# Optimization experiments

Measured on AMD Instinct MI355X. Metric: run time of the kernel, lower is better.

## Reference

```python
import jax, jax.numpy as jnp
import numpy as np

NEG_SLOPE = 0.2
NEG_INF = -1e9


def _gat_branch(x, src, dst, edge_type, t, W, a_src, a_dst, b):
    """Single-head PyG GATConv restricted (by masking) to edges with edge_type == t,
    with self-loops added (PyG default add_self_loops=True)."""
    N = x.shape[0]
    h = x @ W                                   # [N, out_dim]
    s = h @ a_src                               # [N] source attention term
    d = h @ a_dst                               # [N] destination attention term
    # real edges (masked by type)
    e_edge = jax.nn.leaky_relu(s[src] + d[dst], NEG_SLOPE)
    e_edge = jnp.where(edge_type == t, e_edge, NEG_INF)
    # self-loop edges i -> i
    e_self = jax.nn.leaky_relu(s + d, NEG_SLOPE)
    dst_all = jnp.concatenate([dst, jnp.arange(N)])          # [E+N]
    e_all = jnp.concatenate([e_edge, e_self])                 # [E+N]
    # softmax over incoming edges per destination node (segment softmax)
    m = jax.ops.segment_max(e_all, dst_all, num_segments=N)
    p = jnp.exp(e_all - m[dst_all])
    denom = jax.ops.segment_sum(p, dst_all, num_segments=N)
    alpha = p / denom[dst_all]                                 # [E+N]
    msg = jnp.concatenate([h[src], h], axis=0) * alpha[:, None]
    return jax.ops.segment_sum(msg, dst_all, num_segments=N) + b


def setup_inputs() -> dict:
    key = jax.random.key(0)
    ks = jax.random.split(key, 12)
    N, E, in_dim, out_dim = 100000, 1000000, 64, 64
    glorot = (6.0 / (in_dim + out_dim)) ** 0.5
    att = (6.0 / (1 + out_dim)) ** 0.5
    return {
        "x": jax.random.normal(ks[0], (N, in_dim), dtype=jnp.float32),
        "edge_index": jax.random.randint(ks[1], (2, E), 0, N),
        "edge_type": jax.random.randint(ks[2], (E,), 0, 2),
        "W_login": jax.random.uniform(ks[3], (in_dim, out_dim), jnp.float32, -glorot, glorot),
        "a_src_login": jax.random.uniform(ks[4], (out_dim,), jnp.float32, -att, att),
        "a_dst_login": jax.random.uniform(ks[5], (out_dim,), jnp.float32, -att, att),
        "b_login": jnp.zeros((out_dim,), jnp.float32),
        "W_exec": jax.random.uniform(ks[6], (in_dim, out_dim), jnp.float32, -glorot, glorot),
        "a_src_exec": jax.random.uniform(ks[7], (out_dim,), jnp.float32, -att, att),
        "a_dst_exec": jax.random.uniform(ks[8], (out_dim,), jnp.float32, -att, att),
        "b_exec": jnp.zeros((out_dim,), jnp.float32),
    }


def reference(x, edge_index, edge_type, W_login, a_src_login, a_dst_login, b_login,
              W_exec, a_src_exec, a_dst_exec, b_exec):
    src, dst = edge_index[0], edge_index[1]
    out = _gat_branch(x, src, dst, edge_type, 0, W_login, a_src_login, a_dst_login, b_login)
    out = out + _gat_branch(x, src, dst, edge_type, 1, W_exec, a_src_exec, a_dst_exec, b_exec)
    return out
```

## Files before the change

### kernel.cpp

```cpp
#include <hip/hip_runtime.h>

#define D 64
#define CAP 896
#define BINB 256

typedef unsigned short u16;
typedef __attribute__((ext_vector_type(8))) __bf16 bf16x8;
typedef __attribute__((ext_vector_type(4))) float f32x4;

__device__ __forceinline__ float lrelu(float x) { return x > 0.f ? x : 0.2f * x; }
__device__ __forceinline__ u16 f2bf(float f) {
    unsigned u = __float_as_uint(f);
    return (u16)((u + 0x7fffu + ((u >> 16) & 1u)) >> 16);
}
__device__ __forceinline__ float bf2f(u16 v) { return __uint_as_float((unsigned)v << 16); }
__device__ __forceinline__ unsigned pack2(float lo, float hi) {
    return (unsigned)f2bf(lo) | ((unsigned)f2bf(hi) << 16);
}
__device__ __forceinline__ float blo(unsigned u) { return __uint_as_float(u << 16); }
__device__ __forceinline__ float bhi(unsigned u) { return __uint_as_float(u & 0xffff0000u); }

__global__ __launch_bounds__(256) void k_gemm3(
    const float* __restrict__ x,
    const float* __restrict__ W0, const float* __restrict__ as0, const float* __restrict__ ad0,
    const float* __restrict__ W1, const float* __restrict__ as1, const float* __restrict__ ad1,
    u16* __restrict__ hb, float* __restrict__ s_tab, float* __restrict__ d_tab,
    int N, int ntiles)
{
    __shared__ u16 Wb[2][64][64];
    __shared__ u16 Xb[64][72];
    __shared__ float wsd[4][64];

    const int tid = threadIdx.x;

    for (int i = tid; i < 4096; i += 256) {
        const int k = i >> 6, n = i & 63;
        Wb[0][n][k] = f2bf(W0[i]);
        Wb[1][n][k] = f2bf(W1[i]);
    }
    {
        const int k = tid & 63;
        const int v = tid >> 6;
        const float* Ws = (v < 2) ? W0 : W1;
        const float* av = (v == 0) ? as0 : (v == 1) ? ad0 : (v == 2) ? as1 : ad1;
        float q = 0.f;
        for (int n = 0; n < 64; ++n) q = fmaf(Ws[(k << 6) + n], av[n], q);
        wsd[v][k] = q;
    }
    __syncthreads();

    const int lane = tid & 63;
    const int nl = lane & 15, quad = lane >> 4;
    const int wv = tid >> 6;

    bf16x8 bfrag[2][4][2];
#pragma unroll
    for (int br = 0; br < 2; ++br)
#pragma unroll
        for (int t = 0; t < 4; ++t)
#pragma unroll
            for (int h = 0; h < 2; ++h)
                bfrag[br][t][h] = *(const bf16x8*)&Wb[br][t * 16 + nl][h * 32 + quad * 8];

    const int rstage = tid >> 2;
    const int kc = (tid & 3) << 4;

    for (int tile = blockIdx.x; tile < ntiles; tile += gridDim.x) {
        const long n0 = (long)tile << 6;
        __syncthreads();
        {
            long row = n0 + rstage; if (row >= N) row = N - 1;
            const float4* xp = (const float4*)(x + row * D + kc);
            const float4 v0 = xp[0], v1 = xp[1], v2 = xp[2], v3 = xp[3];

            unsigned q[8];
            q[0] = pack2(v0.x, v0.y); q[1] = pack2(v0.z, v0.w);
            q[2] = pack2(v1.x, v1.y); q[3] = pack2(v1.z, v1.w);
            q[4] = pack2(v2.x, v2.y); q[5] = pack2(v2.z, v2.w);
            q[6] = pack2(v3.x, v3.y); q[7] = pack2(v3.z, v3.w);
            *(uint4*)&Xb[rstage][kc]     = make_uint4(q[0], q[1], q[2], q[3]);
            *(uint4*)&Xb[rstage][kc + 8] = make_uint4(q[4], q[5], q[6], q[7]);

            float ps[4];
#pragma unroll
            for (int v = 0; v < 4; ++v) {
                const float4* wp = (const float4*)&wsd[v][kc];
                const float4 wa = wp[0], wb = wp[1], wc = wp[2], wd = wp[3];
                float s = 0.f;
                s = fmaf(v0.x, wa.x, s); s = fmaf(v0.y, wa.y, s);
                s = fmaf(v0.z, wa.z, s); s = fmaf(v0.w, wa.w, s);
                s = fmaf(v1.x, wb.x, s); s = fmaf(v1.y, wb.y, s);
                s = fmaf(v1.z, wb.z, s); s = fmaf(v1.w, wb.w, s);
                s = fmaf(v2.x, wc.x, s); s = fmaf(v2.y, wc.y, s);
                s = fmaf(v2.z, wc.z, s); s = fmaf(v2.w, wc.w, s);
                s = fmaf(v3.x, wd.x, s); s = fmaf(v3.y, wd.y, s);
                s = fmaf(v3.z, wd.z, s); s = fmaf(v3.w, wd.w, s);
                ps[v] = s;
            }
#pragma unroll
            for (int v = 0; v < 4; ++v) {
                ps[v] += __shfl_xor(ps[v], 1, 64);
                ps[v] += __shfl_xor(ps[v], 2, 64);
            }
            const long rw = n0 + rstage;
            if ((tid & 3) == 0 && rw < N) {
                s_tab[(rw << 1)]     = ps[0]; d_tab[(rw << 1)]     = ps[1];
                s_tab[(rw << 1) | 1] = ps[2]; d_tab[(rw << 1) | 1] = ps[3];
            }
        }
        __syncthreads();

        const int rbase = wv << 4;
        const bf16x8 a0 = *(const bf16x8*)&Xb[rbase + nl][quad * 8];
        const bf16x8 a1 = *(const bf16x8*)&Xb[rbase + nl][32 + quad * 8];

        f32x4 acc[2][4];
#pragma unroll
        for (int br = 0; br < 2; ++br)
#pragma unroll
            for (int t = 0; t < 4; ++t) {
                f32x4 c = {0.f, 0.f, 0.f, 0.f};
                c = __builtin_amdgcn_mfma_f32_16x16x32_bf16(a0, bfrag[br][t][0], c, 0, 0, 0);
                c = __builtin_amdgcn_mfma_f32_16x16x32_bf16(a1, bfrag[br][t][1], c, 0, 0, 0);
                acc[br][t] = c;
            }

#pragma unroll
        for (int reg = 0; reg < 4; ++reg) {
            const long row = n0 + rbase + (quad << 2) + reg;
            if (row < N) {
#pragma unroll
                for (int br = 0; br < 2; ++br) {
                    uint2 v;
                    v.x = pack2(acc[br][0][reg], acc[br][1][reg]);
                    v.y = pack2(acc[br][2][reg], acc[br][3][reg]);
                    *(uint2*)(hb + (((row << 1) | br) << 6) + (nl << 2)) = v;
                }
            }
        }
    }
}

__global__ __launch_bounds__(256) void k_bin1(
    const int* __restrict__ src, const int* __restrict__ dst,
    const int* __restrict__ et, int* __restrict__ bktcnt,
    unsigned* __restrict__ bkt, int E, int nbk, int Eseg)
{
    extern __shared__ int cnt_l[];
    const int tid = threadIdx.x;
    for (int i = tid; i < nbk; i += 256) cnt_l[i] = 0;
    __syncthreads();

    const long e0 = (long)blockIdx.x * Eseg;
    const long e1 = min(e0 + (long)Eseg, (long)E);

    long i = e0 + tid;
    for (; i + 256 * 7 < e1; i += 256 * 8) {
        int d[8];
#pragma unroll
        for (int k = 0; k < 8; ++k) d[k] = dst[i + 256 * k];
#pragma unroll
        for (int k = 0; k < 8; ++k) atomicAdd(&cnt_l[d[k] >> 6], 1);
    }
    for (; i < e1; i += 256) atomicAdd(&cnt_l[dst[i] >> 6], 1);
    __syncthreads();

    for (int j = tid; j < nbk; j += 256) {
        const int c = cnt_l[j];
        cnt_l[j] = c ? atomicAdd(bktcnt + j, c) : 0;
    }
    __syncthreads();

    i = e0 + tid;
    for (; i + 256 * 7 < e1; i += 256 * 8) {
        int d[8];
#pragma unroll
        for (int k = 0; k < 8; ++k) d[k] = dst[i + 256 * k];
#pragma unroll
        for (int k = 0; k < 8; ++k) {
            const int bb = d[k] >> 6;
            const long ii = i + 256 * k;
            const int slot = atomicAdd(&cnt_l[bb], 1);
            if (slot < CAP)
                bkt[(long)bb * CAP + slot] =
                    ((unsigned)(d[k] & 63) << 18) | ((unsigned)src[ii] << 1) | (unsigned)et[ii];
        }
    }
    for (; i < e1; i += 256) {
        const int d = dst[i];
        const int bb = d >> 6;
        const int slot = atomicAdd(&cnt_l[bb], 1);
        if (slot < CAP)
            bkt[(long)bb * CAP + slot] =
                ((unsigned)(d & 63) << 18) | ((unsigned)src[i] << 1) | (unsigned)et[i];
    }
}

__global__ __launch_bounds__(512) void k_proc(
    const int* __restrict__ bktcnt, const unsigned* __restrict__ bkt,
    const float* __restrict__ s_tab, const float* __restrict__ d_tab,
    const u16* __restrict__ hb,
    const float* __restrict__ b0, const float* __restrict__ b1,
    float* __restrict__ out, int N)
{
    __shared__ unsigned tok[CAP];
    __shared__ int degl[64];
    __shared__ int curl[64];
    __shared__ float bsum[64];

    const int tid = threadIdx.x;
    const int b = blockIdx.x;
    const int lo = b << 6;
    const int cnt_nodes = min(64, N - lo);
    const int nb = min(bktcnt[b], CAP);

    if (tid < 64) { degl[tid] = 0; bsum[tid] = b0[tid] + b1[tid]; }
    __syncthreads();

    unsigned pr[2];
    int ns = 0;
    for (int i = tid; i < nb; i += 512) {
        const unsigned p = bkt[(long)b * CAP + i];
        pr[ns++] = p;
        atomicAdd(&degl[(p >> 18) & 63], 1);
    }
    __syncthreads();
    if (tid < 64) {
        int v = degl[tid];
        const int orig = v;
#pragma unroll
        for (int o = 1; o < 64; o <<= 1) {
            const int u = __shfl_up(v, o, 64);
            if (tid >= o) v += u;
        }
        curl[tid] = v - orig;
    }
    __syncthreads();
    for (int k = 0, i = tid; k < ns; i += 512, ++k) {
        const unsigned p = pr[k];
        const int s = atomicAdd(&curl[(p >> 18) & 63], 1);
        tok[s] = p & 0x3FFFFu;
    }
    __syncthreads();

    const int lane = tid & 63;
    const int wave = tid >> 6;
    const int q = lane >> 4;
    const int cl = lane & 15;

    for (int ni = wave; ni < cnt_nodes; ni += 8) {
        const int n = lo + ni;
        const int deg = degl[ni];
        const int off = curl[ni] - deg;
        const float d0n = d_tab[(n << 1)];
        const float d1n = d_tab[(n << 1) | 1];

        if (deg <= 62) {
            const int cnt = deg + 2;
            unsigned cmb = 0; unsigned t = 0; float e = 0.f;
            if (lane < deg) {
                cmb = tok[off + lane];
                t = cmb & 1u;
                e = lrelu(s_tab[cmb] + (t ? d1n : d0n));
            } else if (lane == deg)   { cmb = (unsigned)(n << 1);      t = 0; e = lrelu(s_tab[cmb] + d0n); }
            else if (lane == deg + 1) { cmb = (unsigned)(n << 1) | 1u; t = 1; e = lrelu(s_tab[cmb] + d1n); }

            const bool act = lane < cnt;
            const float p = act ? __expf(e) : 0.f;
            float p0 = t ? 0.f : p;
            float p1 = t ? p : 0.f;
#pragma unroll
            for (int o = 32; o; o >>= 1) {
                p0 += __shfl_xor(p0, o, 64);
                p1 += __shfl_xor(p1, o, 64);
            }
            const float a_r = act ? p / (t ? p1 : p0) : 0.f;

            float4 acc = {0.f, 0.f, 0.f, 0.f};
            const int nq = (cnt + 3) >> 2;
            int pp = 0;
            for (; pp + 1 < nq; pp += 2) {
                const int iA = (pp << 2) + q;
                const int iB = iA + 4;
                const int iBc = iB < cnt ? iB : cnt - 1;
                float aA    = __shfl(a_r, iA, 64);
                unsigned cA = __shfl(cmb, iA, 64);
                float aB    = __shfl(a_r, iBc, 64);
                unsigned cB = __shfl(cmb, iBc, 64);
                if (iB >= cnt) aB = 0.f;
                const uint2 uA = *(const uint2*)(hb + ((long)cA << 6) + (cl << 2));
                const uint2 uB = *(const uint2*)(hb + ((long)cB << 6) + (cl << 2));
                acc.x = fmaf(aA, blo(uA.x), acc.x);
                acc.y = fmaf(aA, bhi(uA.x), acc.y);
                acc.z = fmaf(aA, blo(uA.y), acc.z);
                acc.w = fmaf(aA, bhi(uA.y), acc.w);
                acc.x = fmaf(aB, blo(uB.x), acc.x);
                acc.y = fmaf(aB, bhi(uB.x), acc.y);
                acc.z = fmaf(aB, blo(uB.y), acc.z);
                acc.w = fmaf(aB, bhi(uB.y), acc.w);
            }
            if (pp < nq) {
                const int iA = (pp << 2) + q;
                const int iAc = iA < cnt ? iA : cnt - 1;
                float aA    = __shfl(a_r, iAc, 64);
                unsigned cA = __shfl(cmb, iAc, 64);
                if (iA >= cnt) aA = 0.f;
                const uint2 uA = *(const uint2*)(hb + ((long)cA << 6) + (cl << 2));
                acc.x = fmaf(aA, blo(uA.x), acc.x);
                acc.y = fmaf(aA, bhi(uA.x), acc.y);
                acc.z = fmaf(aA, blo(uA.y), acc.z);
                acc.w = fmaf(aA, bhi(uA.y), acc.w);
            }
            acc.x += __shfl_xor(acc.x, 16, 64);
            acc.y += __shfl_xor(acc.y, 16, 64);
            acc.z += __shfl_xor(acc.z, 16, 64);
            acc.w += __shfl_xor(acc.w, 16, 64);
            acc.x += __shfl_xor(acc.x, 32, 64);
            acc.y += __shfl_xor(acc.y, 32, 64);
            acc.z += __shfl_xor(acc.z, 32, 64);
            acc.w += __shfl_xor(acc.w, 32, 64);
            if (lane < 16) {
                float* op = out + ((long)n << 6);
                op[cl]      = acc.x + bsum[cl];
                op[16 + cl] = acc.y + bsum[16 + cl];
                op[32 + cl] = acc.z + bsum[32 + cl];
                op[48 + cl] = acc.w + bsum[48 + cl];
            }
        } else {
            const int oc = ((lane & 3) << 4) + (lane >> 2);
            const float es0 = lrelu(s_tab[(n << 1)] + d0n);
            const float es1 = lrelu(s_tab[(n << 1) | 1] + d1n);
            float p0 = 0.f, p1 = 0.f;
            for (int j = lane; j < deg; j += 64) {
                const unsigned c = tok[off + j];
                const float e = lrelu(s_tab[c] + ((c & 1u) ? d1n : d0n));
                if (c & 1u) p1 += __expf(e); else p0 += __expf(e);
            }
#pragma unroll
            for (int o = 32; o; o >>= 1) {
                p0 += __shfl_xor(p0, o, 64);
                p1 += __shfl_xor(p1, o, 64);
            }
            const float den0 = p0 + __expf(es0);
            const float den1 = p1 + __expf(es1);

            float acc = (__expf(es0) / den0) * bf2f(hb[((long)n << 7) + lane])
                      + (__expf(es1) / den1) * bf2f(hb[((long)n << 7) + 64 + lane]);
            for (int base = 0; base < deg; base += 64) {
                const int j = base + lane;
                unsigned ck = 0; float a = 0.f;
                if (j < deg) {
                    ck = tok[off + j];
                    const float e = lrelu(s_tab[ck] + ((ck & 1u) ? d1n : d0n));
                    a = __expf(e) / ((ck & 1u) ? den1 : den0);
                }
                const int lim = min(64, deg - base);
                for (int jj = 0; jj < lim; ++jj) {
                    const float aj = __shfl(a, jj, 64);
                    const unsigned cj = __shfl(ck, jj, 64);
                    acc = fmaf(aj, bf2f(hb[((long)cj << 6) + lane]), acc);
                }
            }
            out[((long)n << 6) + oc] = acc + bsum[oc];
        }
    }
}

extern "C" void kernel_launch(void* const* d_in, const int* in_sizes, int n_in,
                              void* d_out, int out_size, void* d_ws, size_t ws_size,
                              hipStream_t stream) {
    const float* x   = (const float*)d_in[0];
    const int*   ei  = (const int*)d_in[1];
    const int*   et  = (const int*)d_in[2];
    const float* W0  = (const float*)d_in[3];
    const float* as0 = (const float*)d_in[4];
    const float* ad0 = (const float*)d_in[5];
    const float* b0  = (const float*)d_in[6];
    const float* W1  = (const float*)d_in[7];
    const float* as1 = (const float*)d_in[8];
    const float* ad1 = (const float*)d_in[9];
    const float* b1  = (const float*)d_in[10];
    float* out = (float*)d_out;

    const int N = in_sizes[0] / D;
    const int E = in_sizes[1] / 2;
    const int* src = ei;
    const int* dst = ei + E;

    const int nbk = (N + 63) >> 6;

    char* w = (char*)d_ws;
    u16* hb = (u16*)w;            w += (size_t)2 * N * D * sizeof(u16);
    float* s_tab = (float*)w;     w += (size_t)2 * N * sizeof(float);
    float* d_tab = (float*)w;     w += (size_t)2 * N * sizeof(float);
    int* bktcnt = (int*)w;        w += (size_t)nbk * sizeof(int);
    unsigned* bkt = (unsigned*)w; w += (size_t)nbk * CAP * sizeof(unsigned);

    const int ntiles = (N + 63) / 64;
    const int Eseg = (E + BINB - 1) / BINB;

    hipMemsetAsync(bktcnt, 0, (size_t)nbk * sizeof(int), stream);
    k_gemm3<<<768, 256, 0, stream>>>(x, W0, as0, ad0, W1, as1, ad1,
                                     hb, s_tab, d_tab, N, ntiles);
    k_bin1<<<BINB, 256, (size_t)nbk * sizeof(int), stream>>>(
        src, dst, et, bktcnt, bkt, E, nbk, Eseg);
    k_proc<<<nbk, 512, 0, stream>>>(bktcnt, bkt, s_tab, d_tab, hb, b0, b1, out, N);
}
```

Measured before the change: 195.1 us.

## Fuse GEMM and edge binning into one launch; precompute per-edge softmax weights in LDS

Merges the GEMM and binning kernels into one grid, so binning blocks run alongside GEMM blocks and one launch is saved. The bin histogram is chunked by BINCH, which makes binning blocks rescan their edge segment several times. In k_proc, self-loops become extra tokens, and each edge's exp weight and per-node denominators are computed once into shared memory with atomics. The high-degree path is removed and every node uses the vectorized gather loop. Risks are extra passes over edges during binning and shared-memory atomic contention on the denominators.

```diff
diff --git a/kernel.cpp b/kernel.cpp
--- a/kernel.cpp
+++ b/kernel.cpp
@@ -3,6 +3,8 @@
 #define D 64
 #define CAP 896
 #define BINB 256
+#define GEMMB 768
+#define BINCH 1600
 
 typedef unsigned short u16;
 typedef __attribute__((ext_vector_type(8))) __bf16 bf16x8;
@@ -13,25 +15,95 @@
     unsigned u = __float_as_uint(f);
     return (u16)((u + 0x7fffu + ((u >> 16) & 1u)) >> 16);
 }
-__device__ __forceinline__ float bf2f(u16 v) { return __uint_as_float((unsigned)v << 16); }
 __device__ __forceinline__ unsigned pack2(float lo, float hi) {
     return (unsigned)f2bf(lo) | ((unsigned)f2bf(hi) << 16);
 }
 __device__ __forceinline__ float blo(unsigned u) { return __uint_as_float(u << 16); }
 __device__ __forceinline__ float bhi(unsigned u) { return __uint_as_float(u & 0xffff0000u); }
 
-__global__ __launch_bounds__(256) void k_gemm3(
+struct SG { u16 Wb[2][64][64]; u16 Xb[64][72]; float wsd[4][64]; };
+struct SB { int cnt[BINCH]; };
+
+__global__ __launch_bounds__(256) void k_gb(
     const float* __restrict__ x,
     const float* __restrict__ W0, const float* __restrict__ as0, const float* __restrict__ ad0,
     const float* __restrict__ W1, const float* __restrict__ as1, const float* __restrict__ ad1,
     u16* __restrict__ hb, float* __restrict__ s_tab, float* __restrict__ d_tab,
-    int N, int ntiles)
+    int N, int ntiles,
+    const int* __restrict__ src, const int* __restrict__ dst, const int* __restrict__ et,
+    int* __restrict__ bktcnt, unsigned* __restrict__ bkt, int E, int nbk, int Eseg)
 {
-    __shared__ u16 Wb[2][64][64];
-    __shared__ u16 Xb[64][72];
-    __shared__ float wsd[4][64];
-
+    __shared__ union SM { SG g; SB bn; } sm;
     const int tid = threadIdx.x;
+
+    if (blockIdx.x >= GEMMB) {
+        int* cnt_l = sm.bn.cnt;
+        const int blk = blockIdx.x - GEMMB;
+        const long e0 = (long)blk * Eseg;
+        const long e1 = min(e0 + (long)Eseg, (long)E);
+        for (int base = 0; base < nbk; base += BINCH) {
+            const int lim = min(BINCH, nbk - base);
+            for (int i = tid; i < lim; i += 256) cnt_l[i] = 0;
+            __syncthreads();
+            long i = e0 + tid;
+            for (; i + 256 * 7 < e1; i += 256 * 8) {
+                int d8[8];
+#pragma unroll
+                for (int k = 0; k < 8; ++k) d8[k] = dst[i + 256 * k];
+#pragma unroll
+                for (int k = 0; k < 8; ++k) {
+                    const int bb = (d8[k] >> 6) - base;
+                    if ((unsigned)bb < (unsigned)lim) atomicAdd(&cnt_l[bb], 1);
+                }
+            }
+            for (; i < e1; i += 256) {
+                const int bb = (dst[i] >> 6) - base;
+                if ((unsigned)bb < (unsigned)lim) atomicAdd(&cnt_l[bb], 1);
+            }
+            __syncthreads();
+            for (int j = tid; j < lim; j += 256) {
+                const int c = cnt_l[j];
+                cnt_l[j] = c ? atomicAdd(bktcnt + base + j, c) : 0;
+            }
+            __syncthreads();
+            i = e0 + tid;
+            for (; i + 256 * 7 < e1; i += 256 * 8) {
+                int d8[8], s8[8], t8[8];
+#pragma unroll
+                for (int k = 0; k < 8; ++k) d8[k] = dst[i + 256 * k];
+#pragma unroll
+                for (int k = 0; k < 8; ++k) s8[k] = src[i + 256 * k];
+#pragma unroll
+                for (int k = 0; k < 8; ++k) t8[k] = et[i + 256 * k];
+#pragma unroll
+                for (int k = 0; k < 8; ++k) {
+                    const int bb = (d8[k] >> 6) - base;
+                    if ((unsigned)bb < (unsigned)lim) {
+                        const int slot = atomicAdd(&cnt_l[bb], 1);
+                        if (slot < CAP)
+                            bkt[(long)(base + bb) * CAP + slot] =
+                                ((unsigned)(d8[k] & 63) << 18) | ((unsigned)s8[k] << 1) | (unsigned)t8[k];
+                    }
+                }
+            }
+            for (; i < e1; i += 256) {
+                const int d = dst[i];
+                const int bb = (d >> 6) - base;
+                if ((unsigned)bb < (unsigned)lim) {
+                    const int slot = atomicAdd(&cnt_l[bb], 1);
+                    if (slot < CAP)
+                        bkt[(long)(base + bb) * CAP + slot] =
+                            ((unsigned)(d & 63) << 18) | ((unsigned)src[i] << 1) | (unsigned)et[i];
+                }
+            }
+            __syncthreads();
+        }
+        return;
+    }
+
+    auto& Wb  = sm.g.Wb;
+    auto& Xb  = sm.g.Xb;
+    auto& wsd = sm.g.wsd;
 
     for (int i = tid; i < 4096; i += 256) {
         const int k = i >> 6, n = i & 63;
@@ -65,7 +137,7 @@
     const int rstage = tid >> 2;
     const int kc = (tid & 3) << 4;
 
-    for (int tile = blockIdx.x; tile < ntiles; tile += gridDim.x) {
+    for (int tile = blockIdx.x; tile < ntiles; tile += GEMMB) {
         const long n0 = (long)tile << 6;
         __syncthreads();
         {
@@ -141,61 +213,6 @@
     }
 }
 
-__global__ __launch_bounds__(256) void k_bin1(
-    const int* __restrict__ src, const int* __restrict__ dst,
-    const int* __restrict__ et, int* __restrict__ bktcnt,
-    unsigned* __restrict__ bkt, int E, int nbk, int Eseg)
-{
-    extern __shared__ int cnt_l[];
-    const int tid = threadIdx.x;
-    for (int i = tid; i < nbk; i += 256) cnt_l[i] = 0;
-    __syncthreads();
-
-    const long e0 = (long)blockIdx.x * Eseg;
-    const long e1 = min(e0 + (long)Eseg, (long)E);
-
-    long i = e0 + tid;
-    for (; i + 256 * 7 < e1; i += 256 * 8) {
-        int d[8];
-#pragma unroll
-        for (int k = 0; k < 8; ++k) d[k] = dst[i + 256 * k];
-#pragma unroll
-        for (int k = 0; k < 8; ++k) atomicAdd(&cnt_l[d[k] >> 6], 1);
-    }
-    for (; i < e1; i += 256) atomicAdd(&cnt_l[dst[i] >> 6], 1);
-    __syncthreads();
-
-    for (int j = tid; j < nbk; j += 256) {
-        const int c = cnt_l[j];
-        cnt_l[j] = c ? atomicAdd(bktcnt + j, c) : 0;
-    }
-    __syncthreads();
-
-    i = e0 + tid;
-    for (; i + 256 * 7 < e1; i += 256 * 8) {
-        int d[8];
-#pragma unroll
-        for (int k = 0; k < 8; ++k) d[k] = dst[i + 256 * k];
-#pragma unroll
-        for (int k = 0; k < 8; ++k) {
-            const int bb = d[k] >> 6;
-            const long ii = i + 256 * k;
-            const int slot = atomicAdd(&cnt_l[bb], 1);
-            if (slot < CAP)
-                bkt[(long)bb * CAP + slot] =
-                    ((unsigned)(d[k] & 63) << 18) | ((unsigned)src[ii] << 1) | (unsigned)et[ii];
-        }
-    }
-    for (; i < e1; i += 256) {
-        const int d = dst[i];
-        const int bb = d >> 6;
-        const int slot = atomicAdd(&cnt_l[bb], 1);
-        if (slot < CAP)
-            bkt[(long)bb * CAP + slot] =
-                ((unsigned)(d & 63) << 18) | ((unsigned)src[i] << 1) | (unsigned)et[i];
-    }
-}
-
 __global__ __launch_bounds__(512) void k_proc(
     const int* __restrict__ bktcnt, const unsigned* __restrict__ bkt,
     const float* __restrict__ s_tab, const float* __restrict__ d_tab,
@@ -203,9 +220,11 @@
     const float* __restrict__ b0, const float* __restrict__ b1,
     float* __restrict__ out, int N)
 {
-    __shared__ unsigned tok[CAP];
-    __shared__ int degl[64];
-    __shared__ int curl[64];
+    __shared__ uint2 tok2[CAP + 128];
+    __shared__ int   degl[64];
+    __shared__ int   curl[64];
+    __shared__ float den[128];
+    __shared__ float dl[128];
     __shared__ float bsum[64];
 
     const int tid = threadIdx.x;
@@ -214,11 +233,18 @@
     const int cnt_nodes = min(64, N - lo);
     const int nb = min(bktcnt[b], CAP);
 
-    if (tid < 64) { degl[tid] = 0; bsum[tid] = b0[tid] + b1[tid]; }
-    __syncthreads();
-
-    unsigned pr[2];
-    int ns = 0;
+    if (tid < 64) {
+        degl[tid] = (lo + tid < N) ? 2 : 0;
+        bsum[tid] = b0[tid] + b1[tid];
+    }
+    if (tid < 128) {
+        den[tid] = 0.f;
+        const int n = lo + (tid >> 1);
+        dl[tid] = (n < N) ? d_tab[(n << 1) | (tid & 1)] : 0.f;
+    }
+    __syncthreads();
+
+    unsigned pr[2]; int ns = 0;
     for (int i = tid; i < nb; i += 512) {
         const unsigned p = bkt[(long)b * CAP + i];
         pr[ns++] = p;
@@ -236,10 +262,26 @@
         curl[tid] = v - orig;
     }
     __syncthreads();
+    if (tid < 2 * cnt_nodes) {
+        const int ni = tid >> 1;
+        const int slot = atomicAdd(&curl[ni], 1);
+        tok2[slot].x = ((unsigned)ni << 18) | ((unsigned)((lo + ni) << 1)) | (unsigned)(tid & 1);
+    }
     for (int k = 0, i = tid; k < ns; i += 512, ++k) {
         const unsigned p = pr[k];
-        const int s = atomicAdd(&curl[(p >> 18) & 63], 1);
-        tok[s] = p & 0x3FFFFu;
+        const int slot = atomicAdd(&curl[(p >> 18) & 63], 1);
+        tok2[slot].x = p;
+    }
+    __syncthreads();
+
+    const int T = nb + (cnt_nodes << 1);
+    for (int j = tid; j < T; j += 512) {
+        const unsigned u = tok2[j].x;
+        const int idx = (int)(((u >> 18) << 1) | (u & 1u));
+        const float e = lrelu(s_tab[u & 0x3FFFFu] + dl[idx]);
+        const float p = __expf(e);
+        tok2[j].y = __float_as_uint(p);
+        atomicAdd(&den[idx], p);
     }
     __syncthreads();
 
@@ -249,119 +291,58 @@
     const int cl = lane & 15;
 
     for (int ni = wave; ni < cnt_nodes; ni += 8) {
-        const int n = lo + ni;
-        const int deg = degl[ni];
-        const int off = curl[ni] - deg;
-        const float d0n = d_tab[(n << 1)];
-        const float d1n = d_tab[(n << 1) | 1];
-
-        if (deg <= 62) {
-            const int cnt = deg + 2;
-            unsigned cmb = 0; unsigned t = 0; float e = 0.f;
-            if (lane < deg) {
-                cmb = tok[off + lane];
-                t = cmb & 1u;
-                e = lrelu(s_tab[cmb] + (t ? d1n : d0n));
-            } else if (lane == deg)   { cmb = (unsigned)(n << 1);      t = 0; e = lrelu(s_tab[cmb] + d0n); }
-            else if (lane == deg + 1) { cmb = (unsigned)(n << 1) | 1u; t = 1; e = lrelu(s_tab[cmb] + d1n); }
-
-            const bool act = lane < cnt;
-            const float p = act ? __expf(e) : 0.f;
-            float p0 = t ? 0.f : p;
-            float p1 = t ? p : 0.f;
-#pragma unroll
-            for (int o = 32; o; o >>= 1) {
-                p0 += __shfl_xor(p0, o, 64);
-                p1 += __shfl_xor(p1, o, 64);
-            }
-            const float a_r = act ? p / (t ? p1 : p0) : 0.f;
-
-            float4 acc = {0.f, 0.f, 0.f, 0.f};
-            const int nq = (cnt + 3) >> 2;
-            int pp = 0;
-            for (; pp + 1 < nq; pp += 2) {
-                const int iA = (pp << 2) + q;
-                const int iB = iA + 4;
-                const int iBc = iB < cnt ? iB : cnt - 1;
-                float aA    = __shfl(a_r, iA, 64);
-                unsigned cA = __shfl(cmb, iA, 64);
-                float aB    = __shfl(a_r, iBc, 64);
-                unsigned cB = __shfl(cmb, iBc, 64);
-                if (iB >= cnt) aB = 0.f;
-                const uint2 uA = *(const uint2*)(hb + ((long)cA << 6) + (cl << 2));
-                const uint2 uB = *(const uint2*)(hb + ((long)cB << 6) + (cl << 2));
-                acc.x = fmaf(aA, blo(uA.x), acc.x);
-                acc.y = fmaf(aA, bhi(uA.x), acc.y);
-                acc.z = fmaf(aA, blo(uA.y), acc.z);
-                acc.w = fmaf(aA, bhi(uA.y), acc.w);
-                acc.x = fmaf(aB, blo(uB.x), acc.x);
-                acc.y = fmaf(aB, bhi(uB.x), acc.y);
-                acc.z = fmaf(aB, blo(uB.y), acc.z);
-                acc.w = fmaf(aB, bhi(uB.y), acc.w);
-            }
-            if (pp < nq) {
-                const int iA = (pp << 2) + q;
-                const int iAc = iA < cnt ? iA : cnt - 1;
-                float aA    = __shfl(a_r, iAc, 64);
-                unsigned cA = __shfl(cmb, iAc, 64);
-                if (iA >= cnt) aA = 0.f;
-                const uint2 uA = *(const uint2*)(hb + ((long)cA << 6) + (cl << 2));
-                acc.x = fmaf(aA, blo(uA.x), acc.x);
-                acc.y = fmaf(aA, bhi(uA.x), acc.y);
-                acc.z = fmaf(aA, blo(uA.y), acc.z);
-                acc.w = fmaf(aA, bhi(uA.y), acc.w);
-            }
-            acc.x += __shfl_xor(acc.x, 16, 64);
-            acc.y += __shfl_xor(acc.y, 16, 64);
-            acc.z += __shfl_xor(acc.z, 16, 64);
-            acc.w += __shfl_xor(acc.w, 16, 64);
-            acc.x += __shfl_xor(acc.x, 32, 64);
-            acc.y += __shfl_xor(acc.y, 32, 64);
-            acc.z += __shfl_xor(acc.z, 32, 64);
-            acc.w += __shfl_xor(acc.w, 32, 64);
-            if (lane < 16) {
-                float* op = out + ((long)n << 6);
-                op[cl]      = acc.x + bsum[cl];
-                op[16 + cl] = acc.y + bsum[16 + cl];
-                op[32 + cl] = acc.z + bsum[32 + cl];
-                op[48 + cl] = acc.w + bsum[48 + cl];
-            }
-        } else {
-            const int oc = ((lane & 3) << 4) + (lane >> 2);
-            const float es0 = lrelu(s_tab[(n << 1)] + d0n);
-            const float es1 = lrelu(s_tab[(n << 1) | 1] + d1n);
-            float p0 = 0.f, p1 = 0.f;
-            for (int j = lane; j < deg; j += 64) {
-                const unsigned c = tok[off + j];
-                const float e = lrelu(s_tab[c] + ((c & 1u) ? d1n : d0n));
-                if (c & 1u) p1 += __expf(e); else p0 += __expf(e);
-            }
-#pragma unroll
-            for (int o = 32; o; o >>= 1) {
-                p0 += __shfl_xor(p0, o, 64);
-                p1 += __shfl_xor(p1, o, 64);
-            }
-            const float den0 = p0 + __expf(es0);
-            const float den1 = p1 + __expf(es1);
-
-            float acc = (__expf(es0) / den0) * bf2f(hb[((long)n << 7) + lane])
-                      + (__expf(es1) / den1) * bf2f(hb[((long)n << 7) + 64 + lane]);
-            for (int base = 0; base < deg; base += 64) {
-                const int j = base + lane;
-                unsigned ck = 0; float a = 0.f;
-                if (j < deg) {
-                    ck = tok[off + j];
-                    const float e = lrelu(s_tab[ck] + ((ck & 1u) ? d1n : d0n));
-                    a = __expf(e) / ((ck & 1u) ? den1 : den0);
-                }
-                const int lim = min(64, deg - base);
-                for (int jj = 0; jj < lim; ++jj) {
-                    const float aj = __shfl(a, jj, 64);
-                    const unsigned cj = __shfl(ck, jj, 64);
-                    acc = fmaf(aj, bf2f(hb[((long)cj << 6) + lane]), acc);
-                }
-            }
-            out[((long)n << 6) + oc] = acc + bsum[oc];
+        const int cnt = degl[ni];
+        const int off = curl[ni] - cnt;
+        const float r0 = 1.f / den[(ni << 1)];
+        const float r1 = 1.f / den[(ni << 1) | 1];
+
+        float4 acc = {0.f, 0.f, 0.f, 0.f};
+        const int nq = (cnt + 3) >> 2;
+        int pp = 0;
+        for (; pp + 1 < nq; pp += 2) {
+            const int iA = (pp << 2) + q;
+            const int iB = iA + 4;
+            const uint2 eA = tok2[off + iA];
+            const uint2 eB = tok2[off + (iB < cnt ? iB : cnt - 1)];
+            const float aA = __uint_as_float(eA.y) * ((eA.x & 1u) ? r1 : r0);
+            float aB = __uint_as_float(eB.y) * ((eB.x & 1u) ? r1 : r0);
+            if (iB >= cnt) aB = 0.f;
+            const uint2 uA = *(const uint2*)(hb + ((long)(eA.x & 0x3FFFFu) << 6) + (cl << 2));
+            const uint2 uB = *(const uint2*)(hb + ((long)(eB.x & 0x3FFFFu) << 6) + (cl << 2));
+            acc.x = fmaf(aA, blo(uA.x), acc.x);
+            acc.y = fmaf(aA, bhi(uA.x), acc.y);
+            acc.z = fmaf(aA, blo(uA.y), acc.z);
+            acc.w = fmaf(aA, bhi(uA.y), acc.w);
+            acc.x = fmaf(aB, blo(uB.x), acc.x);
+            acc.y = fmaf(aB, bhi(uB.x), acc.y);
+            acc.z = fmaf(aB, blo(uB.y), acc.z);
+            acc.w = fmaf(aB, bhi(uB.y), acc.w);
+        }
+        if (pp < nq) {
+            const int iA = (pp << 2) + q;
+            const uint2 eA = tok2[off + (iA < cnt ? iA : cnt - 1)];
+            float aA = __uint_as_float(eA.y) * ((eA.x & 1u) ? r1 : r0);
+            if (iA >= cnt) aA = 0.f;
+            const uint2 uA = *(const uint2*)(hb + ((long)(eA.x & 0x3FFFFu) << 6) + (cl << 2));
+            acc.x = fmaf(aA, blo(uA.x), acc.x);
+            acc.y = fmaf(aA, bhi(uA.x), acc.y);
+            acc.z = fmaf(aA, blo(uA.y), acc.z);
+            acc.w = fmaf(aA, bhi(uA.y), acc.w);
+        }
+        acc.x += __shfl_xor(acc.x, 16, 64);
+        acc.y += __shfl_xor(acc.y, 16, 64);
+        acc.z += __shfl_xor(acc.z, 16, 64);
+        acc.w += __shfl_xor(acc.w, 16, 64);
+        acc.x += __shfl_xor(acc.x, 32, 64);
+        acc.y += __shfl_xor(acc.y, 32, 64);
+        acc.z += __shfl_xor(acc.z, 32, 64);
+        acc.w += __shfl_xor(acc.w, 32, 64);
+        if (lane < 16) {
+            float* op = out + ((long)(lo + ni) << 6);
+            op[cl]      = acc.x + bsum[cl];
+            op[16 + cl] = acc.y + bsum[16 + cl];
+            op[32 + cl] = acc.z + bsum[32 + cl];
+            op[48 + cl] = acc.w + bsum[48 + cl];
         }
     }
 }
@@ -400,9 +381,8 @@
     const int Eseg = (E + BINB - 1) / BINB;
 
     hipMemsetAsync(bktcnt, 0, (size_t)nbk * sizeof(int), stream);
-    k_gemm3<<<768, 256, 0, stream>>>(x, W0, as0, ad0, W1, as1, ad1,
-                                     hb, s_tab, d_tab, N, ntiles);
-    k_bin1<<<BINB, 256, (size_t)nbk * sizeof(int), stream>>>(
-        src, dst, et, bktcnt, bkt, E, nbk, Eseg);
+    k_gb<<<GEMMB + BINB, 256, 0, stream>>>(x, W0, as0, ad0, W1, as1, ad1,
+                                           hb, s_tab, d_tab, N, ntiles,
+                                           src, dst, et, bktcnt, bkt, E, nbk, Eseg);
     k_proc<<<nbk, 512, 0, stream>>>(bktcnt, bkt, s_tab, d_tab, hb, b0, b1, out, N);
 }
```

After: 180.4 us. 1.08x faster.
